# Performance work log

Hardware: AMD Instinct MI355X
Metric: run time of the kernel (lower is better)

Reference implementation:

```python
import jax, jax.numpy as jnp
import numpy as np

N = 100000
E = 1600000
F_IN = 3
H = 64


def setup_inputs() -> dict:
    key = jax.random.key(0)
    ks = jax.random.split(key, 12)
    x = jax.random.normal(ks[0], (N, F_IN), dtype=jnp.float32)
    edge_index = jax.random.randint(ks[1], (2, E), 0, N, dtype=jnp.int64)
    def glorot(k, fi, fo):
        s = jnp.sqrt(6.0 / (fi + fo)).astype(jnp.float32)
        return jax.random.uniform(k, (fi, fo), jnp.float32, -s, s)
    return {
        "x": x,
        "edge_index": edge_index,
        "W1": glorot(ks[2], F_IN, H), "b1": jnp.zeros((H,), jnp.float32),
        "W2": glorot(ks[3], H, H),   "b2": jnp.zeros((H,), jnp.float32),
        "W3": glorot(ks[4], H, H),   "b3": jnp.zeros((H,), jnp.float32),
        "Wh": glorot(ks[5], H, 1),   "bh": jnp.zeros((1,), jnp.float32),
    }


def _gcn_conv(x, src, dst, norm, W, b):
    # linear (no bias) -> gather by src -> scale by symmetric norm -> scatter-add to dst -> + bias
    h = x @ W                      # [N, F_out]
    msg = h[src] * norm[:, None]   # [E+N, F_out] (self-loops included)
    out = jax.ops.segment_sum(msg, dst, num_segments=N)
    return out + b


def reference(x, edge_index, W1, b1, W2, b2, W3, b3, Wh, bh):
    # add self-loops (PyG GCNConv default)
    loop = jnp.arange(N, dtype=edge_index.dtype)
    src = jnp.concatenate([edge_index[0], loop])
    dst = jnp.concatenate([edge_index[1], loop])
    # symmetric normalization deg^{-1/2}[src] * deg^{-1/2}[dst]
    deg = jax.ops.segment_sum(jnp.ones_like(dst, dtype=x.dtype), dst, num_segments=N)
    dinv = jnp.where(deg > 0, jax.lax.rsqrt(deg), 0.0)
    norm = dinv[src] * dinv[dst]

    h = _gcn_conv(x, src, dst, norm, W1, b1)
    h = jax.nn.relu(h)  # dropout is identity in eval mode
    h = _gcn_conv(h, src, dst, norm, W2, b2)
    h = jax.nn.relu(h)
    h = _gcn_conv(h, src, dst, norm, W3, b3)
    logits = (h @ Wh + bh).squeeze(-1)  # [N]
    return logits
```

## Files before the change

### kernel.cpp

```cpp
#include <hip/hip_runtime.h>


#define BKSH 8
#define EPB  4096
#define PAYCAP 192

__device__ __forceinline__ float rlane(float v, int l) {
    return __int_as_float(__builtin_amdgcn_readlane(__float_as_int(v), l));
}
__device__ __forceinline__ int rlane_i(int v, int l) {
    return __builtin_amdgcn_readlane(v, l);
}

__global__ void bhist(const int* __restrict__ dst, int* __restrict__ ghist,
                      int E, int NBK, int BLK) {
    __shared__ int h[512];
    int t = threadIdx.x, b = blockIdx.x;
    for (int i = t; i < NBK; i += 256) h[i] = 0;
    __syncthreads();
    int base = b * EPB;
    #pragma unroll
    for (int i = 0; i < 16; ++i) {
        int e = base + i * 256 + t;
        if (e < E) atomicAdd(&h[dst[e] >> BKSH], 1);
    }
    __syncthreads();
    for (int i = t; i < NBK; i += 256) ghist[(size_t)i * BLK + b] = h[i];
}

__global__ void gscan1(const int* __restrict__ in, int* __restrict__ out,
                       int* __restrict__ bsums, int M) {
    __shared__ int tmp[256];
    int i = blockIdx.x * 256 + threadIdx.x;
    int v = (i < M) ? in[i] : 0;
    tmp[threadIdx.x] = v; __syncthreads();
    for (int off = 1; off < 256; off <<= 1) {
        int t = (threadIdx.x >= off) ? tmp[threadIdx.x - off] : 0;
        __syncthreads();
        tmp[threadIdx.x] += t;
        __syncthreads();
    }
    if (i < M) out[i] = tmp[threadIdx.x] - v;
    if (threadIdx.x == 255) bsums[blockIdx.x] = tmp[255];
}

__global__ void gscan2(int* __restrict__ bsums, int nb) {
    __shared__ int tmp[1024];
    int v = (threadIdx.x < nb) ? bsums[threadIdx.x] : 0;
    tmp[threadIdx.x] = v; __syncthreads();
    for (int off = 1; off < 1024; off <<= 1) {
        int t = (threadIdx.x >= off) ? tmp[threadIdx.x - off] : 0;
        __syncthreads();
        tmp[threadIdx.x] += t;
        __syncthreads();
    }
    if (threadIdx.x < nb) bsums[threadIdx.x] = tmp[threadIdx.x] - v;
}

__global__ void bscatter(const int* __restrict__ src, const int* __restrict__ dst,
                         const int* __restrict__ goff, const int* __restrict__ gbsums,
                         unsigned* __restrict__ tmp, int E, int NBK, int BLK) {
    __shared__ int off[512];
    int t = threadIdx.x, b = blockIdx.x;
    for (int i = t; i < NBK; i += 256) {
        size_t m = (size_t)i * BLK + b;
        off[i] = goff[m] + gbsums[m >> 8];
    }
    __syncthreads();
    int base = b * EPB;
    #pragma unroll
    for (int i = 0; i < 16; ++i) {
        int e = base + i * 256 + t;
        if (e < E) {
            int d = dst[e];
            int p = atomicAdd(&off[d >> BKSH], 1);
            tmp[p] = ((unsigned)src[e] << 8) | (unsigned)(d & 255);
        }
    }
}

__global__ void bucketAF(const unsigned* __restrict__ tmp, const int* __restrict__ goff,
                         const int* __restrict__ gbsums, const float* __restrict__ x,
                         int* __restrict__ rowptr, float* __restrict__ dinv,
                         float4* __restrict__ xd4, int* __restrict__ ewsrc,
                         int N, int NBK, int BLK, int E) {
    __shared__ int lc[256], sc[256], rbase[256];
    int b = blockIdx.x, t = threadIdx.x;
    lc[t] = 0; __syncthreads();
    size_t m0 = (size_t)b * BLK;
    int p0 = goff[m0] + gbsums[m0 >> 8];
    int p1 = E;
    if (b + 1 < NBK) { size_t m1 = (size_t)(b + 1) * BLK; p1 = goff[m1] + gbsums[m1 >> 8]; }
    for (int p = p0 + t; p < p1; p += 256) atomicAdd(&lc[tmp[p] & 255u], 1);
    __syncthreads();
    int v = lc[t];
    sc[t] = v; __syncthreads();
    for (int off = 1; off < 256; off <<= 1) {
        int tv = (t >= off) ? sc[t - off] : 0;
        __syncthreads();
        sc[t] += tv;
        __syncthreads();
    }
    int rb = p0 + (sc[t] - v);
    rbase[t] = rb;
    int node = (b << BKSH) + t;
    if (node < N) {
        rowptr[node] = rb;
        float dvv = rsqrtf((float)(v + 1));
        dinv[node] = dvv;
        xd4[node]  = make_float4(dvv * x[3*node], dvv * x[3*node+1],
                                 dvv * x[3*node+2], 0.f);
    }
    if (b == 0 && t == 0) rowptr[N] = E;
    lc[t] = 0;
    __syncthreads();
    for (int p = p0 + t; p < p1; p += 256) {
        unsigned e = tmp[p];
        int dl = (int)(e & 255u);
        int pos = rbase[dl] + atomicAdd(&lc[dl], 1);
        ewsrc[pos] = (int)(e >> 8);
    }
}

__global__ void agg3w(const int* __restrict__ ewsrc, const int* __restrict__ rowptr,
                      const float* __restrict__ dinv, const float4* __restrict__ xd4,
                      float4* __restrict__ a1,
                      const float* __restrict__ W3, const float* __restrict__ b3,
                      const float* __restrict__ Wh, const float* __restrict__ bh,
                      float* __restrict__ wc, int N) {
    if (blockIdx.x == 0 && threadIdx.x < 64) {
        int k = threadIdx.x;
        float accw = 0.f;
        for (int f = 0; f < 64; f++) accw += W3[k*64+f] * Wh[f];
        wc[k] = accw;
        if (k == 0) {
            float bb = bh[0];
            for (int f = 0; f < 64; f++) bb += b3[f] * Wh[f];
            wc[64] = bb;
        }
    }
    int g   = (blockIdx.x * blockDim.x + threadIdx.x) >> 4;
    int sub = threadIdx.x & 15;
    if (g >= N) return;
    int p0 = rowptr[g], p1 = rowptr[g+1];
    float ax = 0.f, ay = 0.f, az = 0.f;
    for (int p = p0 + sub; p < p1; p += 16) {
        float4 xs = xd4[ewsrc[p]];
        ax += xs.x; ay += xs.y; az += xs.z;
    }
    #pragma unroll
    for (int off = 8; off; off >>= 1) {
        ax += __shfl_down(ax, off, 16);
        ay += __shfl_down(ay, off, 16);
        az += __shfl_down(az, off, 16);
    }
    if (sub == 0) {
        float dv = dinv[g];
        float4 xn = xd4[g];
        a1[g] = make_float4(dv * (ax + xn.x), dv * (ay + xn.y),
                            dv * (az + xn.z), dv);
    }
}

__global__ void fused_l2l3(const int* __restrict__ ewsrc, const int* __restrict__ rowptr,
                           const float4* __restrict__ a1, const float* __restrict__ W1,
                           const float* __restrict__ b1, const float* __restrict__ W2,
                           const float* __restrict__ b2, const float* __restrict__ wc,
                           float* __restrict__ zz, int N, int E) {
    __shared__ float  Wl[64*64];
    __shared__ float4 pay[4][PAYCAP];
    __shared__ float  a2buf[4][64];
    const int tid = threadIdx.x;
    for (int i = tid; i < 4096; i += 256) Wl[i] = W2[i];
    const int lane = tid & 63;
    const int wv   = tid >> 6;
    const float w10 = W1[lane], w11 = W1[64+lane], w12 = W1[128+lane];
    const float b1f = b1[lane], b2f = b2[lane], wcf = wc[lane];
    const int NPW = 8;
    const int n0 = (blockIdx.x * 4 + wv) * NPW;
    int   rpl = rowptr[min(n0 + lane, N)];
    float4 sg = a1[min(n0 + lane, N - 1)];
    __syncthreads();
    if (n0 >= N) return;
    int NPWv = N - n0; if (NPWv > NPW) NPWv = NPW;
    const int P0 = rlane_i(rpl, 0);
    const int P8 = rlane_i(rpl, NPWv);
    int span  = P8 - P0;
    int stage = span < PAYCAP ? span : PAYCAP;
    for (int w = 0; w < stage; w += 64) {
        int idx = w + lane;
        if (idx < stage) pay[wv][idx] = a1[ewsrc[P0 + idx]];
    }
    for (int cur = 0; cur < NPWv; ++cur) {
        int p0 = rlane_i(rpl, cur);
        int p1 = rlane_i(rpl, cur + 1);
        float sx = rlane(sg.x, cur), sy = rlane(sg.y, cur);
        float sz2 = rlane(sg.z, cur), sw = rlane(sg.w, cur);
        float ts = fmaf(sz2, w12, fmaf(sy, w11, fmaf(sx, w10, b1f)));
        float acc0 = sw * fmaxf(ts, 0.f);
        float acc1 = 0.f, acc2 = 0.f, acc3 = 0.f;
        {
            int js  = p0 - P0;
            int jse = p1 - P0; if (jse > stage) jse = stage;
            const float4* pp = (const float4*)&pay[wv][0];
            int j = js;
            for (; j + 3 < jse; j += 4) {
                float4 Q0 = pp[j], Q1 = pp[j+1], Q2 = pp[j+2], Q3 = pp[j+3];
                float t0 = fmaf(Q0.z, w12, fmaf(Q0.y, w11, fmaf(Q0.x, w10, b1f)));
                float t1 = fmaf(Q1.z, w12, fmaf(Q1.y, w11, fmaf(Q1.x, w10, b1f)));
                float t2 = fmaf(Q2.z, w12, fmaf(Q2.y, w11, fmaf(Q2.x, w10, b1f)));
                float t3 = fmaf(Q3.z, w12, fmaf(Q3.y, w11, fmaf(Q3.x, w10, b1f)));
                acc0 = fmaf(Q0.w, fmaxf(t0, 0.f), acc0);
                acc1 = fmaf(Q1.w, fmaxf(t1, 0.f), acc1);
                acc2 = fmaf(Q2.w, fmaxf(t2, 0.f), acc2);
                acc3 = fmaf(Q3.w, fmaxf(t3, 0.f), acc3);
            }
            for (; j < jse; ++j) {
                float4 Q = pp[j];
                float tt = fmaf(Q.z, w12, fmaf(Q.y, w11, fmaf(Q.x, w10, b1f)));
                acc1 = fmaf(Q.w, fmaxf(tt, 0.f), acc1);
            }
        }
        int ov = P0 + stage; if (ov < p0) ov = p0;
        for (int pc = ov; pc < p1; pc += 64) {
            int pidx = pc + lane; if (pidx >= p1) pidx = p1 - 1;
            float4 g2 = a1[ewsrc[pidx]];
            pay[wv][lane] = g2;
            int m2 = p1 - pc; if (m2 > 64) m2 = 64;
            const float4* pp = (const float4*)&pay[wv][0];
            for (int jj = 0; jj < m2; ++jj) {
                float4 Q = pp[jj];
                float tt = fmaf(Q.z, w12, fmaf(Q.y, w11, fmaf(Q.x, w10, b1f)));
                acc2 = fmaf(Q.w, fmaxf(tt, 0.f), acc2);
            }
        }
        float acc = ((acc0 + acc1) + (acc2 + acc3)) * sw;
        a2buf[wv][lane] = acc;
        float ha = 0.f, hb = 0.f, hc = 0.f, hd = 0.f;
        const float4* a4 = (const float4*)&a2buf[wv][0];
        #pragma unroll
        for (int k4 = 0; k4 < 16; ++k4) {
            float4 a = a4[k4];
            ha = fmaf(a.x, Wl[(4*k4+0)*64 + lane], ha);
            hb = fmaf(a.y, Wl[(4*k4+1)*64 + lane], hb);
            hc = fmaf(a.z, Wl[(4*k4+2)*64 + lane], hc);
            hd = fmaf(a.w, Wl[(4*k4+3)*64 + lane], hd);
        }
        float h = b2f + ((ha + hb) + (hc + hd));
        float v = fmaxf(h, 0.f) * wcf;
        #pragma unroll
        for (int off = 32; off; off >>= 1) v += __shfl_down(v, off);
        if (lane == 0) zz[n0 + cur] = sw * v;
    }
}

__global__ void final_wave(const float* __restrict__ zz, const int* __restrict__ ewsrc,
                           const int* __restrict__ rowptr, const float* __restrict__ dinv,
                           const float* __restrict__ wc, float* __restrict__ out, int N) {
    int g   = (blockIdx.x * blockDim.x + threadIdx.x) >> 4;
    int sub = threadIdx.x & 15;
    if (g >= N) return;
    int p0 = rowptr[g], p1 = rowptr[g+1];
    float acc = 0.f;
    for (int p = p0 + sub; p < p1; p += 16) {
        acc += zz[ewsrc[p]];
    }
    #pragma unroll
    for (int off = 8; off; off >>= 1) acc += __shfl_down(acc, off, 16);
    if (sub == 0) {
        out[g] = fmaf(dinv[g], zz[g] + acc, wc[64]);
    }
}

extern "C" void kernel_launch(void* const* d_in, const int* in_sizes, int n_in,
                              void* d_out, int out_size, void* d_ws, size_t ws_size,
                              hipStream_t stream) {
    const float* x   = (const float*)d_in[0];
    const int*   ei  = (const int*)d_in[1];
    const float* W1  = (const float*)d_in[2];
    const float* b1  = (const float*)d_in[3];
    const float* W2  = (const float*)d_in[4];
    const float* b2  = (const float*)d_in[5];
    const float* W3  = (const float*)d_in[6];
    const float* b3  = (const float*)d_in[7];
    const float* Wh  = (const float*)d_in[8];
    const float* bh  = (const float*)d_in[9];
    float* logits = (float*)d_out;

    const int N = in_sizes[0] / 3;
    const int E = in_sizes[1] / 2;
    const int* src = ei;
    const int* dst = ei + E;

    const int NBK = (N + 255) >> BKSH;
    const int BLK = (E + EPB - 1) / EPB;
    const int M   = NBK * BLK;

    float* base = (float*)d_ws;
    size_t o = 0;
    float*    dinv   = base + o; o += (size_t)N;
    o = (o + 3) & ~(size_t)3;
    float4*   a1     = (float4*)(base + o); o += (size_t)4*N;
    float4*   xd4    = (float4*)(base + o); o += (size_t)4*N;
    int*      rowptr = (int*)(base + o); o += (size_t)N + 1;
    int*      gbsums = (int*)(base + o); o += 1024;
    int*      ewsrc  = (int*)(base + o); o += (size_t)E;
    unsigned* tmpp   = (unsigned*)(base + o); o += (size_t)E;
    float*    zz     = base + o; o += (size_t)N;
    float*    wc     = base + o; o += 65;
    int*      ghist  = (int*)(base + o); o += (size_t)M;
    int*      goff   = (int*)(base + o); o += (size_t)M;

    const int BS = 256;
    int gM   = (M + BS - 1) / BS;
    int g16  = ((size_t)N * 16 + BS - 1) / BS;
    int gFU  = (N + 31) / 32;

    bhist    <<<BLK, BS, 0, stream>>>(dst, ghist, E, NBK, BLK);
    gscan1   <<<gM,  BS, 0, stream>>>(ghist, goff, gbsums, M);
    gscan2   <<<1, 1024, 0, stream>>>(gbsums, gM);
    bscatter <<<BLK, BS, 0, stream>>>(src, dst, goff, gbsums, tmpp, E, NBK, BLK);
    bucketAF <<<NBK, BS, 0, stream>>>(tmpp, goff, gbsums, x, rowptr, dinv, xd4, ewsrc, N, NBK, BLK, E);
    agg3w    <<<g16, BS, 0, stream>>>(ewsrc, rowptr, dinv, xd4, a1, W3, b3, Wh, bh, wc, N);

    fused_l2l3 <<<gFU, BS, 0, stream>>>(ewsrc, rowptr, a1, W1, b1, W2, b2, wc, zz, N, E);
    final_wave <<<g16, BS, 0, stream>>>(zz, ewsrc, rowptr, dinv, wc, logits, N);
}
```

Measured before the change: 132.2 us.

## Split fused layer-2 aggregation and 64x64 matmul into separate kernels

The fused kernel that aggregated layer-2 features and then applied the 64x64 weight matrix per node is split into two kernels. The aggregation kernel writes a 64-wide intermediate per node to a new global buffer, and a second kernel loads W2 into LDS and does the matmul, ReLU and dot with wc. The aim is to drop the 16 KB of LDS for W2 from the gather kernel, which should raise its occupancy and remove its block-wide sync. The cost is writing and rereading about 25 MB of intermediate data plus an extra launch.

```diff
diff --git a/kernel.cpp b/kernel.cpp
--- a/kernel.cpp
+++ b/kernel.cpp
@@ -162,26 +162,21 @@
     }
 }
 
-__global__ void fused_l2l3(const int* __restrict__ ewsrc, const int* __restrict__ rowptr,
-                           const float4* __restrict__ a1, const float* __restrict__ W1,
-                           const float* __restrict__ b1, const float* __restrict__ W2,
-                           const float* __restrict__ b2, const float* __restrict__ wc,
-                           float* __restrict__ zz, int N, int E) {
-    __shared__ float  Wl[64*64];
+__global__ void aggA(const int* __restrict__ ewsrc, const int* __restrict__ rowptr,
+                     const float4* __restrict__ a1, const float* __restrict__ W1,
+                     const float* __restrict__ b1, float* __restrict__ a2,
+                     int N, int E) {
     __shared__ float4 pay[4][PAYCAP];
-    __shared__ float  a2buf[4][64];
     const int tid = threadIdx.x;
-    for (int i = tid; i < 4096; i += 256) Wl[i] = W2[i];
     const int lane = tid & 63;
     const int wv   = tid >> 6;
     const float w10 = W1[lane], w11 = W1[64+lane], w12 = W1[128+lane];
-    const float b1f = b1[lane], b2f = b2[lane], wcf = wc[lane];
+    const float b1f = b1[lane];
     const int NPW = 8;
     const int n0 = (blockIdx.x * 4 + wv) * NPW;
+    if (n0 >= N) return;
     int   rpl = rowptr[min(n0 + lane, N)];
     float4 sg = a1[min(n0 + lane, N - 1)];
-    __syncthreads();
-    if (n0 >= N) return;
     int NPWv = N - n0; if (NPWv > NPW) NPWv = NPW;
     const int P0 = rlane_i(rpl, 0);
     const int P8 = rlane_i(rpl, NPWv);
@@ -235,22 +230,42 @@
             }
         }
         float acc = ((acc0 + acc1) + (acc2 + acc3)) * sw;
-        a2buf[wv][lane] = acc;
-        float ha = 0.f, hb = 0.f, hc = 0.f, hd = 0.f;
-        const float4* a4 = (const float4*)&a2buf[wv][0];
+        a2[(size_t)(n0 + cur) * 64 + lane] = acc;
+    }
+}
+
+__global__ void mm64z(const float* __restrict__ a2, const float* __restrict__ W2,
+                      const float* __restrict__ b2, const float* __restrict__ wc,
+                      const float* __restrict__ dinv, float* __restrict__ zz, int N) {
+    __shared__ float Wl[64*64];
+    __shared__ float bl[64];
+    int tid = threadIdx.x;
+    for (int i = tid; i < 4096; i += 256) Wl[i] = W2[i];
+    if (tid < 64) bl[tid] = b2[tid];
+    __syncthreads();
+    const int f = tid & 63;
+    const int g = tid >> 6;
+    const float wcf = wc[f];
+    const int NPT = 8;
+    int base = blockIdx.x * (4 * NPT);
+    const float4* A4 = (const float4*)a2;
+    #pragma unroll
+    for (int i = 0; i < NPT; i++) {
+        int n = base + g + 4*i;
+        if (n >= N) continue;
+        float ha = bl[f], hb = 0.f, hc = 0.f, hd = 0.f;
         #pragma unroll
-        for (int k4 = 0; k4 < 16; ++k4) {
-            float4 a = a4[k4];
-            ha = fmaf(a.x, Wl[(4*k4+0)*64 + lane], ha);
-            hb = fmaf(a.y, Wl[(4*k4+1)*64 + lane], hb);
-            hc = fmaf(a.z, Wl[(4*k4+2)*64 + lane], hc);
-            hd = fmaf(a.w, Wl[(4*k4+3)*64 + lane], hd);
-        }
-        float h = b2f + ((ha + hb) + (hc + hd));
-        float v = fmaxf(h, 0.f) * wcf;
+        for (int k4 = 0; k4 < 16; k4++) {
+            float4 a = A4[(size_t)n*16 + k4];
+            ha = fmaf(a.x, Wl[(4*k4+0)*64 + f], ha);
+            hb = fmaf(a.y, Wl[(4*k4+1)*64 + f], hb);
+            hc = fmaf(a.z, Wl[(4*k4+2)*64 + f], hc);
+            hd = fmaf(a.w, Wl[(4*k4+3)*64 + f], hd);
+        }
+        float v = fmaxf((ha + hb) + (hc + hd), 0.f) * wcf;
         #pragma unroll
         for (int off = 32; off; off >>= 1) v += __shfl_down(v, off);
-        if (lane == 0) zz[n0 + cur] = sw * v;
+        if (f == 0) zz[n] = dinv[n] * v;
     }
 }
 
@@ -310,6 +325,8 @@
     float*    wc     = base + o; o += 65;
     int*      ghist  = (int*)(base + o); o += (size_t)M;
     int*      goff   = (int*)(base + o); o += (size_t)M;
+    o = (o + 3) & ~(size_t)3;
+    float*    a2g    = base + o; o += (size_t)64*N;
 
     const int BS = 256;
     int gM   = (M + BS - 1) / BS;
@@ -323,6 +340,7 @@
     bucketAF <<<NBK, BS, 0, stream>>>(tmpp, goff, gbsums, x, rowptr, dinv, xd4, ewsrc, N, NBK, BLK, E);
     agg3w    <<<g16, BS, 0, stream>>>(ewsrc, rowptr, dinv, xd4, a1, W3, b3, Wh, bh, wc, N);
 
-    fused_l2l3 <<<gFU, BS, 0, stream>>>(ewsrc, rowptr, a1, W1, b1, W2, b2, wc, zz, N, E);
+    aggA     <<<gFU, BS, 0, stream>>>(ewsrc, rowptr, a1, W1, b1, a2g, N, E);
+    mm64z    <<<gFU, BS, 0, stream>>>(a2g, W2, b2, wc, dinv, zz, N);
     final_wave <<<g16, BS, 0, stream>>>(zz, ewsrc, rowptr, dinv, wc, logits, N);
 }
```

Measured after the change: 157.3 us. 19.0% more time.

## Enlarge edges per block and fold block-sum scan into consumer kernels

Applied to the files above, without the earlier changes.

Raises the number of edges handled per histogram and scatter block from 4096 to 16384, which shrinks the histogram matrix, the number of scan blocks and the global offset traffic. With the matrix smaller, the second-level scan (gscan2) is removed and each bscatter and bucketAF block instead rescans the block sums redundantly in shared memory, saving one kernel launch. The trade-off is fewer blocks in bhist and bscatter, about 98 for 1.6M edges, which may underfill the GPU, plus extra per-block scan work. The local scan only handles up to 256 block sums, so it is correct only while gM stays at or below 256.

```diff
diff --git a/kernel.cpp b/kernel.cpp
--- a/kernel.cpp
+++ b/kernel.cpp
@@ -2,7 +2,7 @@
 
 
 #define BKSH 8
-#define EPB  4096
+#define EPB  16384
 #define PAYCAP 192
 
 __device__ __forceinline__ float rlane(float v, int l) {
@@ -19,11 +19,8 @@
     for (int i = t; i < NBK; i += 256) h[i] = 0;
     __syncthreads();
     int base = b * EPB;
-    #pragma unroll
-    for (int i = 0; i < 16; ++i) {
-        int e = base + i * 256 + t;
-        if (e < E) atomicAdd(&h[dst[e] >> BKSH], 1);
-    }
+    int end  = base + EPB; if (end > E) end = E;
+    for (int e = base + t; e < end; e += 256) atomicAdd(&h[dst[e] >> BKSH], 1);
     __syncthreads();
     for (int i = t; i < NBK; i += 256) ghist[(size_t)i * BLK + b] = h[i];
 }
@@ -44,53 +41,57 @@
     if (threadIdx.x == 255) bsums[blockIdx.x] = tmp[255];
 }
 
-__global__ void gscan2(int* __restrict__ bsums, int nb) {
-    __shared__ int tmp[1024];
-    int v = (threadIdx.x < nb) ? bsums[threadIdx.x] : 0;
-    tmp[threadIdx.x] = v; __syncthreads();
-    for (int off = 1; off < 1024; off <<= 1) {
-        int t = (threadIdx.x >= off) ? tmp[threadIdx.x - off] : 0;
-        __syncthreads();
-        tmp[threadIdx.x] += t;
-        __syncthreads();
-    }
-    if (threadIdx.x < nb) bsums[threadIdx.x] = tmp[threadIdx.x] - v;
+__device__ __forceinline__ void scan_bsums(const int* __restrict__ bsums, int gM,
+                                           int* sgb , int t) {
+    int v = (t < gM) ? bsums[t] : 0;
+    sgb[t] = v; __syncthreads();
+    for (int off = 1; off < 256; off <<= 1) {
+        int tv = (t >= off) ? sgb[t - off] : 0;
+        __syncthreads();
+        sgb[t] += tv;
+        __syncthreads();
+    }
+    int excl = sgb[t] - v;
+    __syncthreads();
+    sgb[t] = excl;
+    __syncthreads();
 }
 
 __global__ void bscatter(const int* __restrict__ src, const int* __restrict__ dst,
-                         const int* __restrict__ goff, const int* __restrict__ gbsums,
-                         unsigned* __restrict__ tmp, int E, int NBK, int BLK) {
+                         const int* __restrict__ goff, const int* __restrict__ bsums,
+                         int gM, unsigned* __restrict__ tmp, int E, int NBK, int BLK) {
     __shared__ int off[512];
+    __shared__ int sgb[256];
     int t = threadIdx.x, b = blockIdx.x;
+    scan_bsums(bsums, gM, sgb, t);
     for (int i = t; i < NBK; i += 256) {
         size_t m = (size_t)i * BLK + b;
-        off[i] = goff[m] + gbsums[m >> 8];
+        off[i] = goff[m] + sgb[m >> 8];
     }
     __syncthreads();
     int base = b * EPB;
-    #pragma unroll
-    for (int i = 0; i < 16; ++i) {
-        int e = base + i * 256 + t;
-        if (e < E) {
-            int d = dst[e];
-            int p = atomicAdd(&off[d >> BKSH], 1);
-            tmp[p] = ((unsigned)src[e] << 8) | (unsigned)(d & 255);
-        }
+    int end  = base + EPB; if (end > E) end = E;
+    for (int e = base + t; e < end; e += 256) {
+        int d = dst[e];
+        int p = atomicAdd(&off[d >> BKSH], 1);
+        tmp[p] = ((unsigned)src[e] << 8) | (unsigned)(d & 255);
     }
 }
 
 __global__ void bucketAF(const unsigned* __restrict__ tmp, const int* __restrict__ goff,
-                         const int* __restrict__ gbsums, const float* __restrict__ x,
+                         const int* __restrict__ bsums, int gM, const float* __restrict__ x,
                          int* __restrict__ rowptr, float* __restrict__ dinv,
                          float4* __restrict__ xd4, int* __restrict__ ewsrc,
                          int N, int NBK, int BLK, int E) {
     __shared__ int lc[256], sc[256], rbase[256];
+    __shared__ int sgb[256];
     int b = blockIdx.x, t = threadIdx.x;
+    scan_bsums(bsums, gM, sgb, t);
     lc[t] = 0; __syncthreads();
     size_t m0 = (size_t)b * BLK;
-    int p0 = goff[m0] + gbsums[m0 >> 8];
+    int p0 = goff[m0] + sgb[m0 >> 8];
     int p1 = E;
-    if (b + 1 < NBK) { size_t m1 = (size_t)(b + 1) * BLK; p1 = goff[m1] + gbsums[m1 >> 8]; }
+    if (b + 1 < NBK) { size_t m1 = (size_t)(b + 1) * BLK; p1 = goff[m1] + sgb[m1 >> 8]; }
     for (int p = p0 + t; p < p1; p += 256) atomicAdd(&lc[tmp[p] & 255u], 1);
     __syncthreads();
     int v = lc[t];
@@ -295,6 +296,7 @@
     const int NBK = (N + 255) >> BKSH;
     const int BLK = (E + EPB - 1) / EPB;
     const int M   = NBK * BLK;
+    const int gM  = (M + 255) / 256;
 
     float* base = (float*)d_ws;
     size_t o = 0;
@@ -303,7 +305,7 @@
     float4*   a1     = (float4*)(base + o); o += (size_t)4*N;
     float4*   xd4    = (float4*)(base + o); o += (size_t)4*N;
     int*      rowptr = (int*)(base + o); o += (size_t)N + 1;
-    int*      gbsums = (int*)(base + o); o += 1024;
+    int*      bsums  = (int*)(base + o); o += 1024;
     int*      ewsrc  = (int*)(base + o); o += (size_t)E;
     unsigned* tmpp   = (unsigned*)(base + o); o += (size_t)E;
     float*    zz     = base + o; o += (size_t)N;
@@ -312,15 +314,13 @@
     int*      goff   = (int*)(base + o); o += (size_t)M;
 
     const int BS = 256;
-    int gM   = (M + BS - 1) / BS;
     int g16  = ((size_t)N * 16 + BS - 1) / BS;
     int gFU  = (N + 31) / 32;
 
     bhist    <<<BLK, BS, 0, stream>>>(dst, ghist, E, NBK, BLK);
-    gscan1   <<<gM,  BS, 0, stream>>>(ghist, goff, gbsums, M);
-    gscan2   <<<1, 1024, 0, stream>>>(gbsums, gM);
-    bscatter <<<BLK, BS, 0, stream>>>(src, dst, goff, gbsums, tmpp, E, NBK, BLK);
-    bucketAF <<<NBK, BS, 0, stream>>>(tmpp, goff, gbsums, x, rowptr, dinv, xd4, ewsrc, N, NBK, BLK, E);
+    gscan1   <<<gM,  BS, 0, stream>>>(ghist, goff, bsums, M);
+    bscatter <<<BLK, BS, 0, stream>>>(src, dst, goff, bsums, gM, tmpp, E, NBK, BLK);
+    bucketAF <<<NBK, BS, 0, stream>>>(tmpp, goff, bsums, gM, x, rowptr, dinv, xd4, ewsrc, N, NBK, BLK, E);
     agg3w    <<<g16, BS, 0, stream>>>(ewsrc, rowptr, dinv, xd4, a1, W3, b3, Wh, bh, wc, N);
 
     fused_l2l3 <<<gFU, BS, 0, stream>>>(ewsrc, rowptr, a1, W1, b1, W2, b2, wc, zz, N, E);
```

New measurement: 162.1 us. 22.6% more time.
